# Optimization experiments

Measured on AMD Instinct MI355X. Metric: run time of the kernel, lower is better.

The kernel has to match this reference:

```python
import jax, jax.numpy as jnp
import numpy as np

V = 100000   # number of node ids in the embedding table
D = 128      # embedding dim
B = 8192     # batch of target nodes
K = 32       # fixed neighbor count per node


def setup_inputs() -> dict:
    key = jax.random.key(0)
    k1, k2 = jax.random.split(key)
    neigh_ids = jax.random.randint(k1, (B, K), 0, V, dtype=jnp.int64)
    embed = jax.random.normal(k2, (V, D), dtype=jnp.float32)  # id2feat table
    return {"neigh_ids": neigh_ids, "embed": embed}


def reference(neigh_ids, embed):
    # Original: build dense normalized one-hot mask [B, n_unique] and mm with
    # gathered unique embeddings. That is exactly the per-row mean of the
    # neighbors' embeddings (neighbors are sets -> no duplicates per row).
    neigh_feats = jnp.take(embed, neigh_ids, axis=0)  # [B, K, D] gather
    return jnp.mean(neigh_feats, axis=1)              # [B, D]
```

## Files before the change

### kernel.cpp

```cpp
#include <hip/hip_runtime.h>
#include <hip/hip_bf16.h>


#define K_NEIGH 32
#define D4      32
#define ROWS_PER_BLOCK 8

__global__ __launch_bounds__(256) void mean_agg_kernel(
    const int* __restrict__ ids,
    const float4* __restrict__ embed,
    float4* __restrict__ out)
{
    const int tid = threadIdx.x;
    const int row = blockIdx.x * ROWS_PER_BLOCK + (tid >> 5);
    const int c   = tid & 31;

    const int my_id = ids[row * K_NEIGH + c];

    float4 acc = make_float4(0.f, 0.f, 0.f, 0.f);

#pragma unroll
    for (int k = 0; k < K_NEIGH; ++k) {
        const int id = __shfl(my_id, k, 32);
        const float4 v = embed[(long)id * D4 + c];
        acc.x += v.x; acc.y += v.y; acc.z += v.z; acc.w += v.w;
    }

    const float s = 1.0f / (float)K_NEIGH;
    acc.x *= s; acc.y *= s; acc.z *= s; acc.w *= s;
    out[row * D4 + c] = acc;
}

extern "C" void kernel_launch(void* const* d_in, const int* in_sizes, int n_in,
                              void* d_out, int out_size, void* d_ws, size_t ws_size,
                              hipStream_t stream) {
    const int*    ids   = (const int*)d_in[0];
    const float4* embed = (const float4*)d_in[1];
    float4*       out   = (float4*)d_out;

    const int B = 8192;
    dim3 grid(B / ROWS_PER_BLOCK);
    dim3 block(256);
    mean_agg_kernel<<<grid, block, 0, stream>>>(ids, embed, out);
}
```

Baseline: 96.07 us.

## Map one row per wavefront with float2 lanes and scalar neighbor ids

Each 64-lane wavefront now handles one output row, with each lane loading a float2, instead of two rows per wave using float4. The row index is made wave-uniform so the 32 neighbor ids can be read through scalar loads instead of cross-lane shuffles. The gathers are issued in batches of 16 before accumulation to keep more loads in flight, and launch bounds request higher occupancy. The risks are that narrower 8-byte loads issue more memory instructions per byte and the grid doubles in block count.

Measured after the change: 96.04 us. Within noise of the previous version (-0.0%).

```diff
diff --git a/kernel.cpp b/kernel.cpp
--- a/kernel.cpp
+++ b/kernel.cpp
@@ -3,40 +3,51 @@
 
 
 #define K_NEIGH 32
-#define D4      32
-#define ROWS_PER_BLOCK 8
+#define D2      64
+#define ROWS_PER_BLOCK 4
+#define BATCH 16
 
-__global__ __launch_bounds__(256) void mean_agg_kernel(
+__global__ __launch_bounds__(256, 4) void mean_agg_kernel(
     const int* __restrict__ ids,
-    const float4* __restrict__ embed,
-    float4* __restrict__ out)
+    const float2* __restrict__ embed,
+    float2* __restrict__ out)
 {
-    const int tid = threadIdx.x;
-    const int row = blockIdx.x * ROWS_PER_BLOCK + (tid >> 5);
-    const int c   = tid & 31;
+    const int lane = threadIdx.x & 63;
+    int row = blockIdx.x * ROWS_PER_BLOCK + (threadIdx.x >> 6);
+    row = __builtin_amdgcn_readfirstlane(row);
 
-    const int my_id = ids[row * K_NEIGH + c];
+    const int* __restrict__ rowids = ids + row * K_NEIGH;
+    int sid[K_NEIGH];
+#pragma unroll
+    for (int k = 0; k < K_NEIGH; ++k) sid[k] = rowids[k];
 
-    float4 acc = make_float4(0.f, 0.f, 0.f, 0.f);
+    float2 acc = make_float2(0.f, 0.f);
 
 #pragma unroll
-    for (int k = 0; k < K_NEIGH; ++k) {
-        const int id = __shfl(my_id, k, 32);
-        const float4 v = embed[(long)id * D4 + c];
-        acc.x += v.x; acc.y += v.y; acc.z += v.z; acc.w += v.w;
+    for (int half = 0; half < K_NEIGH / BATCH; ++half) {
+        float2 v[BATCH];
+#pragma unroll
+        for (int j = 0; j < BATCH; ++j) {
+            const int id = sid[half * BATCH + j];
+            v[j] = embed[(long)id * D2 + lane];
+        }
+#pragma unroll
+        for (int j = 0; j < BATCH; ++j) {
+            acc.x += v[j].x;
+            acc.y += v[j].y;
+        }
     }
 
     const float s = 1.0f / (float)K_NEIGH;
-    acc.x *= s; acc.y *= s; acc.z *= s; acc.w *= s;
-    out[row * D4 + c] = acc;
+    out[row * D2 + lane] = make_float2(acc.x * s, acc.y * s);
 }
 
 extern "C" void kernel_launch(void* const* d_in, const int* in_sizes, int n_in,
                               void* d_out, int out_size, void* d_ws, size_t ws_size,
                               hipStream_t stream) {
     const int*    ids   = (const int*)d_in[0];
-    const float4* embed = (const float4*)d_in[1];
-    float4*       out   = (float4*)d_out;
+    const float2* embed = (const float2*)d_in[1];
+    float2*       out   = (float2*)d_out;
 
     const int B = 8192;
     dim3 grid(B / ROWS_PER_BLOCK);
```
